# Performance work log

Measured on AMD Instinct MI355X. Metric: run time of the kernel, lower is better.

The kernel has to match this reference:

```python
import jax, jax.numpy as jnp
import numpy as np

EPS = 1e-8


def setup_inputs() -> dict:
    key = jax.random.key(0)
    k1, k2 = jax.random.split(key)
    N, D, K = 200000, 256, 64
    embeds = jax.random.normal(k1, (N, D), dtype=jnp.float32)
    init = jax.random.uniform(k2, (K, D), dtype=jnp.float32)  # torch.rand(K, n_h)
    beta = jnp.ones((1,), dtype=jnp.float32)
    return {"embeds": embeds, "init": init, "beta": beta, "num_iter": 11}


def reference(embeds, init, beta, num_iter):
    # embeds: [N, D], init: [K, D], beta: scalar temperature
    data_abs = jnp.linalg.norm(embeds, axis=1, keepdims=True)            # [N, 1]
    data_norm = embeds / jnp.maximum(data_abs, EPS)                      # [N, D]
    b = beta.reshape(())
    mu = init
    r = None
    for _ in range(num_iter):  # small fixed iteration count (default 11)
        mu_abs = jnp.linalg.norm(mu, axis=1, keepdims=True)              # [K, 1]
        mu_norm = mu / jnp.maximum(mu_abs, EPS)                          # [K, D]
        dist = data_norm @ mu_norm.T                                     # [N, K]
        r = jax.nn.softmax(b * dist, axis=1)                             # [N, K]
        cluster_r = r.sum(axis=0)                                        # [K]
        cluster_mean = r.T @ embeds                                      # [K, D]
        mu = cluster_mean / cluster_r[:, None]                           # diag(1/cluster_r) @ cluster_mean
    return mu, r
```

## Files before the change

### kernel.cpp

```cpp
#include <hip/hip_runtime.h>
#include <math.h>


#define N_ROWS 200000
#define DIM 256
#define KC 64
#define NUM_ITER 11
#define TR 64
#define NTILES (N_ROWS / TR)
#define EPSV 1e-8f
#define NB 256

typedef _Float16 half8 __attribute__((ext_vector_type(8)));
typedef _Float16 half4 __attribute__((ext_vector_type(4)));
typedef float f32x4 __attribute__((ext_vector_type(4)));

typedef __attribute__((address_space(3))) void as3_void;
typedef __attribute__((address_space(1))) void as1_void;

__device__ __forceinline__ void glds16(const void* g, void* l) {
  __builtin_amdgcn_global_load_lds((const as1_void*)g, (as3_void*)l, 16, 0, 0);
}

__device__ __forceinline__ float wave_reduce_sum(float v) {
#pragma unroll
  for (int off = 32; off > 0; off >>= 1) v += __shfl_xor(v, off, 64);
  return v;
}

__device__ __forceinline__ void barrier_lgkm_only() {
  __builtin_amdgcn_sched_barrier(0);
  asm volatile("s_waitcnt lgkmcnt(0)" ::: "memory");
  __builtin_amdgcn_s_barrier();
  __builtin_amdgcn_sched_barrier(0);
}


__global__ void rn_convert_kernel(const float* __restrict__ embeds,
                                  float* __restrict__ inv_norm,
                                  _Float16* __restrict__ Xh) {
  int gw = (blockIdx.x * blockDim.x + threadIdx.x) >> 6;
  int lane = threadIdx.x & 63;
  int nw = (gridDim.x * blockDim.x) >> 6;
  for (int row = gw; row < N_ROWS; row += nw) {
    float4 v = *(const float4*)(embeds + (size_t)row * DIM + 4 * lane);
    float s = v.x * v.x;
    s = fmaf(v.y, v.y, s); s = fmaf(v.z, v.z, s); s = fmaf(v.w, v.w, s);
    s = wave_reduce_sum(s);
    if (lane == 0) inv_norm[row] = 1.0f / fmaxf(sqrtf(s), EPSV);
    half4 h;
    h[0] = (_Float16)v.x; h[1] = (_Float16)v.y; h[2] = (_Float16)v.z; h[3] = (_Float16)v.w;
    *(half4*)(Xh + (size_t)row * DIM + 4 * lane) = h;
  }
}

__global__ void prep0_raw(const float* __restrict__ init, float* __restrict__ mu_raw,
                          float* __restrict__ mu_ssq) {
  int k = blockIdx.x, lane = threadIdx.x;
  float4 v = *(const float4*)(init + (size_t)k * DIM + 4 * lane);
  *(float4*)(mu_raw + (size_t)k * DIM + 4 * lane) = v;
  float s = v.x * v.x;
  s = fmaf(v.y, v.y, s); s = fmaf(v.z, v.z, s); s = fmaf(v.w, v.w, s);
#pragma unroll
  for (int off = 1; off < 16; off <<= 1) s += __shfl_xor(s, off, 64);
  if ((lane & 15) == 0) mu_ssq[k * 4 + (lane >> 4)] = s;
}

__device__ __forceinline__ void stage_row512_8(const _Float16* g, _Float16* l,
                                               int wid, int lane) {
#pragma unroll
  for (int ii = 0; ii < 4; ++ii) {
    int i = wid * 4 + ii;
    int row = i * 2 + (lane >> 5);
    int slot = (lane & 31) ^ (row & 7);
    glds16((const char*)g + row * 512 + slot * 16, (char*)l + i * 1024);
  }
}

template <int LAST>
__global__ __launch_bounds__(512, 2) void cluster_main8(
    const _Float16* __restrict__ Xh, const float* __restrict__ inv_norm,
    const float* __restrict__ beta, const float* __restrict__ mu_raw,
    const float* __restrict__ mu_ssq, float* __restrict__ part_cm,
    float* __restrict__ part_crt, float* __restrict__ r_out) {
  __shared__ alignas(16) _Float16 mu_lds[KC * DIM];
  __shared__ alignas(16) _Float16 x_lds[2][TR * DIM];
  __shared__ alignas(16) _Float16 xt_lds[DIM * TR];
  __shared__ alignas(16) _Float16 r_lds[KC * TR];
  __shared__ f32x4 dist_lds[16 * 64];
  __shared__ float cr_lds[4 * KC];

  const int tid = threadIdx.x, wid = tid >> 6, lane = tid & 63;
  const int l15 = lane & 15, h = lane >> 4;
  const int kh = wid >> 2, rg = wid & 3;
  const float b = beta[0];
  const int myrow = 16 * rg + l15;
  const int rb0 = blockIdx.x;

  stage_row512_8(Xh + (size_t)rb0 * TR * DIM, x_lds[0], wid, lane);

  if (tid < KC) {
    const float4 s4 = *(const float4*)&mu_ssq[4 * tid];
    cr_lds[tid] = 1.0f / fmaxf(sqrtf(s4.x + s4.y + s4.z + s4.w), EPSV);
  }
  __syncthreads();
  {
    const float4* mu_raw4 = (const float4*)mu_raw;
#pragma unroll
    for (int i = 0; i < 8; ++i) {
      const int idx = tid + 512 * i;
      const int cl = idx >> 6;
      const int dim0 = (idx & 63) * 4;
      float4 v = mu_raw4[idx];
      const float iv = cr_lds[cl];
      const int sw = dim0 ^ ((cl & 7) << 3);
      half4 hh;
      hh[0] = (_Float16)(v.x * iv); hh[1] = (_Float16)(v.y * iv);
      hh[2] = (_Float16)(v.z * iv); hh[3] = (_Float16)(v.w * iv);
      *(half4*)&mu_lds[cl * DIM + sw] = hh;
    }
  }
  f32x4 acc2[4][2] = {};
  float cr_acc[16] = {};
  __syncthreads();

  int p = 0;
  for (int rb = rb0; rb < NTILES; rb += NB, p ^= 1) {
    const int row0 = rb * TR;
    const int rbn = rb + NB;
    if (rbn < NTILES)
      stage_row512_8(Xh + (size_t)rbn * TR * DIM, x_lds[p ^ 1], wid, lane);

    f32x4 acc1[4] = {};
    const _Float16* xb = x_lds[p];
#pragma unroll
    for (int t = 0; t < 4; ++t) {
      const int kb = 128 * kh + 32 * t + 8 * h;
      half8 bx = *(const half8*)&xb[myrow * DIM + (kb ^ ((myrow & 7) << 3))];
#pragma unroll
      for (int m = 0; m < 4; ++m) {
        const int cl = 16 * m + l15;
        half8 am = *(const half8*)&mu_lds[cl * DIM + (kb ^ ((cl & 7) << 3))];
        acc1[m] = __builtin_amdgcn_mfma_f32_16x16x32_f16(am, bx, acc1[m], 0, 0, 0);
      }
    }
    if (kh) {
#pragma unroll
      for (int m = 0; m < 4; ++m) dist_lds[(rg * 4 + m) * 64 + lane] = acc1[m];
    }
    barrier_lgkm_only();

    if (!kh) {
#pragma unroll
      for (int m = 0; m < 4; ++m) {
        f32x4 o = dist_lds[(rg * 4 + m) * 64 + lane];
        acc1[m] += o;
      }
      const int xr = row0 + myrow;
      const float sc = b * inv_norm[xr];
#pragma unroll
      for (int m = 0; m < 4; ++m)
#pragma unroll
        for (int j = 0; j < 4; ++j) acc1[m][j] *= sc;
      float mx = -1e30f;
#pragma unroll
      for (int m = 0; m < 4; ++m)
#pragma unroll
        for (int j = 0; j < 4; ++j) mx = fmaxf(mx, acc1[m][j]);
      mx = fmaxf(mx, __shfl_xor(mx, 16));
      mx = fmaxf(mx, __shfl_xor(mx, 32));
      float esum = 0.f;
#pragma unroll
      for (int m = 0; m < 4; ++m)
#pragma unroll
        for (int j = 0; j < 4; ++j) {
          float e = __expf(acc1[m][j] - mx);
          acc1[m][j] = e;
          esum += e;
        }
      esum += __shfl_xor(esum, 16);
      esum += __shfl_xor(esum, 32);
      const float rcp = 1.0f / esum;
#pragma unroll
      for (int m = 0; m < 4; ++m) {
#pragma unroll
        for (int j = 0; j < 4; ++j) {
          const float rv = acc1[m][j] * rcp;
          acc1[m][j] = rv;
          const int cl = 16 * m + 4 * h + j;
          cr_acc[m * 4 + j] += rv;
          r_lds[cl * TR + (myrow ^ ((cl & 7) << 3))] = (_Float16)rv;
        }
        if (LAST)
          *(float4*)&r_out[(size_t)xr * KC + 16 * m + 4 * h] = *(float4*)&acc1[m];
      }
    } else {
      const int t8 = tid & 255;
      const int db = t8 >> 3;
      const int rb8 = t8 & 7;
      union U { uint4 v; unsigned u[4]; };
      U tin[8];
#pragma unroll
      for (int k2 = 0; k2 < 8; ++k2)
        tin[k2].v = *(const uint4*)&xb[(8 * rb8 + k2) * DIM + ((8 * db) ^ (k2 << 3))];
#pragma unroll
      for (int j = 0; j < 8; ++j) {
        const unsigned sel = (j & 1) ? 0x07060302u : 0x05040100u;
        U o;
#pragma unroll
        for (int m2 = 0; m2 < 4; ++m2)
          o.u[m2] = __builtin_amdgcn_perm(tin[2 * m2 + 1].u[j >> 1],
                                          tin[2 * m2].u[j >> 1], sel);
        *(uint4*)&xt_lds[(8 * db + j) * TR + 8 * (rb8 ^ j)] = o.v;
      }
    }

    barrier_lgkm_only();

#pragma unroll
    for (int t = 0; t < 2; ++t) {
      const int kb = 32 * t + 8 * h;
      half8 ar[4], bx2[2];
#pragma unroll
      for (int m = 0; m < 4; ++m) {
        const int cl = 16 * m + l15;
        ar[m] = *(const half8*)&r_lds[cl * TR + (kb ^ ((cl & 7) << 3))];
      }
#pragma unroll
      for (int n = 0; n < 2; ++n) {
        const int dm = 32 * wid + 16 * n + l15;
        bx2[n] = *(const half8*)&xt_lds[dm * TR + (kb ^ ((dm & 7) << 3))];
      }
#pragma unroll
      for (int m = 0; m < 4; ++m)
#pragma unroll
        for (int n = 0; n < 2; ++n)
          acc2[m][n] = __builtin_amdgcn_mfma_f32_16x16x32_f16(ar[m], bx2[n], acc2[m][n], 0, 0, 0);
    }
    __syncthreads();
  }

  float* pc = part_cm + (size_t)blockIdx.x * (KC * DIM);
#pragma unroll
  for (int m = 0; m < 4; ++m)
#pragma unroll
    for (int n = 0; n < 2; ++n)
#pragma unroll
      for (int j = 0; j < 4; ++j)
        pc[(16 * m + 4 * h + j) * DIM + 32 * wid + 16 * n + l15] = acc2[m][n][j];
  if (wid < 4) {
#pragma unroll
    for (int m = 0; m < 4; ++m)
#pragma unroll
      for (int j = 0; j < 4; ++j) {
        float v = cr_acc[m * 4 + j];
        v += __shfl_xor(v, 1); v += __shfl_xor(v, 2);
        v += __shfl_xor(v, 4); v += __shfl_xor(v, 8);
        if (l15 == 0) cr_lds[wid * KC + 16 * m + 4 * h + j] = v;
      }
  }
  __syncthreads();
  if (wid == 0)
    part_crt[(size_t)lane * NB + blockIdx.x] =
        cr_lds[lane] + cr_lds[KC + lane] + cr_lds[2 * KC + lane] + cr_lds[3 * KC + lane];
}

template <int FINAL>
__global__ void reduce_mu(const float* __restrict__ part_cm,
                          const float* __restrict__ part_crt,
                          float* __restrict__ mu_raw, float* __restrict__ mu_ssq,
                          float* __restrict__ mu_out) {
  const int cl = blockIdx.x, q = blockIdx.y;
  const int tid = threadIdx.x, wid = tid >> 6, lane = tid & 63;
  __shared__ float red2[4 * 64];
  __shared__ float cr4[4];
  float c = part_crt[(size_t)cl * NB + tid];
  c = wave_reduce_sum(c);
  if (lane == 0) cr4[wid] = c;
  float s = 0.f;
  const float* basep =
      part_cm + (size_t)(64 * wid) * (KC * DIM) + cl * DIM + 64 * q + lane;
#pragma unroll 8
  for (int i = 0; i < 64; ++i) s += basep[(size_t)i * (KC * DIM)];
  red2[wid * 64 + lane] = s;
  __syncthreads();
  if (wid == 0) {
    const float crv = cr4[0] + cr4[1] + cr4[2] + cr4[3];
    const float st = red2[lane] + red2[64 + lane] + red2[128 + lane] + red2[192 + lane];
    const float mu = st / crv;
    const int dim = 64 * q + lane;
    if (FINAL) {
      mu_out[cl * DIM + dim] = mu;
    } else {
      mu_raw[cl * DIM + dim] = mu;
      float ss = wave_reduce_sum(mu * mu);
      if (lane == 0) mu_ssq[cl * 4 + q] = ss;
    }
  }
}

__global__ void rownorm_v1(const float* __restrict__ embeds, float* __restrict__ inv_norm) {
  int gw = (blockIdx.x * blockDim.x + threadIdx.x) >> 6;
  int lane = threadIdx.x & 63;
  int nw = (gridDim.x * blockDim.x) >> 6;
  for (int row = gw; row < N_ROWS; row += nw) {
    const float* rp = embeds + (size_t)row * DIM;
    float s = 0.f;
#pragma unroll
    for (int j = 0; j < 4; ++j) { float v = rp[lane + 64 * j]; s = fmaf(v, v, s); }
    s = wave_reduce_sum(s);
    if (lane == 0) inv_norm[row] = 1.0f / fmaxf(sqrtf(s), EPSV);
  }
}
__global__ void prep0_v1(const float* __restrict__ init, float* __restrict__ muT) {
  int k = blockIdx.x, lane = threadIdx.x;
  const float* rp = init + k * DIM;
  float v[4]; float s = 0.f;
#pragma unroll
  for (int j = 0; j < 4; ++j) { v[j] = rp[lane + 64 * j]; s = fmaf(v[j], v[j], s); }
  s = wave_reduce_sum(s);
  float inv = 1.0f / fmaxf(sqrtf(s), EPSV);
#pragma unroll
  for (int j = 0; j < 4; ++j) muT[(lane + 64 * j) * KC + k] = v[j] * inv;
}
__device__ __forceinline__ float wave_reduce_max_v1(float v) {
#pragma unroll
  for (int off = 32; off > 0; off >>= 1) v = fmaxf(v, __shfl_xor(v, off, 64));
  return v;
}
template <int LAST>
__global__ __launch_bounds__(256, 1) void main_v1(
    const float* __restrict__ embeds, const float* __restrict__ inv_norm,
    const float* __restrict__ muT, const float* __restrict__ beta,
    float* __restrict__ part_cm, float* __restrict__ part_cr,
    float* __restrict__ r_out, int nb) {
  __shared__ float mu_l[DIM * KC];
  __shared__ float x_l[TR * DIM];
  __shared__ float r_l[TR * KC];
  __shared__ float cr_l[4 * KC];
  const int tid = threadIdx.x, wid = tid >> 6, lane = tid & 63;
  const float b = beta[0];
  {
    const float4* m4 = (const float4*)muT; float4* ml4 = (float4*)mu_l;
#pragma unroll
    for (int i = 0; i < 16; ++i) ml4[tid + i * 256] = m4[tid + i * 256];
  }
  float acc[64];
#pragma unroll
  for (int i = 0; i < 64; ++i) acc[i] = 0.f;
  float cr = 0.f;
  for (int rb = blockIdx.x; rb < NTILES; rb += nb) {
    const int row0 = rb * TR;
    __syncthreads();
    {
      const float4* x4 = (const float4*)(embeds + (size_t)row0 * DIM);
      float4* xl4 = (float4*)x_l;
#pragma unroll
      for (int i = 0; i < 16; ++i) xl4[tid + i * 256] = x4[tid + i * 256];
    }
    __syncthreads();
    float dist[16];
#pragma unroll
    for (int r = 0; r < 16; ++r) dist[r] = 0.f;
    const int rbase = wid * 16;
    for (int d = 0; d < DIM; d += 4) {
      float mv0 = mu_l[(d + 0) * KC + lane], mv1 = mu_l[(d + 1) * KC + lane];
      float mv2 = mu_l[(d + 2) * KC + lane], mv3 = mu_l[(d + 3) * KC + lane];
#pragma unroll
      for (int r = 0; r < 16; ++r) {
        float4 xv = *(const float4*)&x_l[(rbase + r) * DIM + d];
        dist[r] = fmaf(xv.x, mv0, dist[r]); dist[r] = fmaf(xv.y, mv1, dist[r]);
        dist[r] = fmaf(xv.z, mv2, dist[r]); dist[r] = fmaf(xv.w, mv3, dist[r]);
      }
    }
#pragma unroll
    for (int r = 0; r < 16; ++r) {
      const int row = rbase + r;
      float s = b * (dist[r] * inv_norm[row0 + row]);
      float m = wave_reduce_max_v1(s);
      float e = __expf(s - m);
      float sum = wave_reduce_sum(e);
      float rv = e * (1.0f / sum);
      cr += rv;
      r_l[row * KC + lane] = rv;
      if (LAST) r_out[(size_t)(row0 + row) * KC + lane] = rv;
    }
    __syncthreads();
    const int dbase = wid * 64;
    for (int row = 0; row < TR; ++row) {
      float rv = r_l[row * KC + lane];
#pragma unroll
      for (int dd = 0; dd < 64; dd += 4) {
        float4 xv = *(const float4*)&x_l[row * DIM + dbase + dd];
        acc[dd + 0] = fmaf(rv, xv.x, acc[dd + 0]); acc[dd + 1] = fmaf(rv, xv.y, acc[dd + 1]);
        acc[dd + 2] = fmaf(rv, xv.z, acc[dd + 2]); acc[dd + 3] = fmaf(rv, xv.w, acc[dd + 3]);
      }
    }
  }
  {
    float* pp = part_cm + ((size_t)blockIdx.x * KC + lane) * DIM + wid * 64;
#pragma unroll
    for (int dd = 0; dd < 64; dd += 4)
      *(float4*)&pp[dd] = make_float4(acc[dd], acc[dd + 1], acc[dd + 2], acc[dd + 3]);
    cr_l[wid * KC + lane] = cr;
  }
  __syncthreads();
  if (wid == 0) {
    float c = cr_l[lane] + cr_l[64 + lane] + cr_l[128 + lane] + cr_l[192 + lane];
    part_cr[(size_t)blockIdx.x * KC + lane] = c;
  }
}
template <int FINAL>
__global__ void reduce_v1(const float* __restrict__ part_cm, const float* __restrict__ part_cr,
                          float* __restrict__ muT, float* __restrict__ mu_out, int nb) {
  const int k = blockIdx.x, t = threadIdx.x;
  __shared__ float red[256];
  float s = 0.f;
  for (int bl = 0; bl < nb; ++bl) s += part_cm[((size_t)bl * KC + k) * DIM + t];
  float c = 0.f;
  for (int bl = t; bl < nb; bl += 256) c += part_cr[(size_t)bl * KC + k];
  red[t] = c; __syncthreads();
#pragma unroll
  for (int off = 128; off > 0; off >>= 1) { if (t < off) red[t] += red[t + off]; __syncthreads(); }
  const float crv = red[0]; __syncthreads();
  const float mu = s / crv;
  if (FINAL) { mu_out[k * DIM + t] = mu; return; }
  red[t] = mu * mu; __syncthreads();
#pragma unroll
  for (int off = 128; off > 0; off >>= 1) { if (t < off) red[t] += red[t + off]; __syncthreads(); }
  const float inv = 1.0f / fmaxf(sqrtf(red[0]), EPSV);
  muT[t * KC + k] = mu * inv;
}

extern "C" void kernel_launch(void* const* d_in, const int* in_sizes, int n_in,
                              void* d_out, int out_size, void* d_ws, size_t ws_size,
                              hipStream_t stream) {
  const float* embeds = (const float*)d_in[0];
  const float* init = (const float*)d_in[1];
  const float* beta = (const float*)d_in[2];
  float* out_mu = (float*)d_out;
  float* out_r = out_mu + KC * DIM;
  char* ws = (char*)d_ws;

  const size_t szX = (size_t)N_ROWS * DIM * 2;
  const size_t szInv = (size_t)N_ROWS * 4;
  const size_t szMuR = (size_t)KC * DIM * 4;
  const size_t szSsq = (size_t)KC * 4 * 4;
  const size_t szPC = (size_t)NB * KC * DIM * 4;
  const size_t szPR = (size_t)KC * NB * 4;
  const size_t need = szX + szInv + szMuR + szSsq + szPC + szPR;

  if (ws_size >= need) {
    char* pp = ws;
    _Float16* Xh = (_Float16*)pp; pp += szX;
    float* invn = (float*)pp; pp += szInv;
    float* mu_raw = (float*)pp; pp += szMuR;
    float* mu_ssq = (float*)pp; pp += szSsq;
    float* pcm = (float*)pp; pp += szPC;
    float* pcrt = (float*)pp;

    rn_convert_kernel<<<2048, 256, 0, stream>>>(embeds, invn, Xh);
    prep0_raw<<<KC, 64, 0, stream>>>(init, mu_raw, mu_ssq);
    for (int it = 0; it < NUM_ITER; ++it) {
      if (it > 0)
        reduce_mu<0><<<dim3(KC, 4), 256, 0, stream>>>(pcm, pcrt, mu_raw, mu_ssq, nullptr);
      if (it == NUM_ITER - 1)
        cluster_main8<1><<<NB, 512, 0, stream>>>(Xh, invn, beta, mu_raw, mu_ssq,
                                                 pcm, pcrt, out_r);
      else
        cluster_main8<0><<<NB, 512, 0, stream>>>(Xh, invn, beta, mu_raw, mu_ssq,
                                                 pcm, pcrt, out_r);
    }
    reduce_mu<1><<<dim3(KC, 4), 256, 0, stream>>>(pcm, pcrt, nullptr, nullptr, out_mu);
  } else {
    float* wsf = (float*)d_ws;
    float* muT = wsf;
    float* invn = muT + DIM * KC;
    size_t avail = ws_size / sizeof(float);
    size_t fixed = (size_t)DIM * KC + N_ROWS;
    size_t per_blk = (size_t)KC * DIM + KC;
    int nb = 256;
    if (avail > fixed) {
      size_t mx = (avail - fixed) / per_blk;
      if (mx < 256) nb = (int)mx;
    } else nb = 1;
    if (nb < 1) nb = 1;
    float* pcm = invn + N_ROWS;
    float* pcr = pcm + (size_t)nb * KC * DIM;

    rownorm_v1<<<2048, 256, 0, stream>>>(embeds, invn);
    prep0_v1<<<KC, 64, 0, stream>>>(init, muT);
    for (int it = 0; it < NUM_ITER; ++it) {
      if (it > 0) reduce_v1<0><<<KC, 256, 0, stream>>>(pcm, pcr, muT, nullptr, nb);
      if (it == NUM_ITER - 1)
        main_v1<1><<<nb, 256, 0, stream>>>(embeds, invn, muT, beta, pcm, pcr, out_r, nb);
      else
        main_v1<0><<<nb, 256, 0, stream>>>(embeds, invn, muT, beta, pcm, pcr, nullptr, nb);
    }
    reduce_v1<1><<<KC, 256, 0, stream>>>(pcm, pcr, muT, out_mu, nb);
  }
}
```

Measured before the change: 517.0 us.

## Triple-buffer X tiles, transpose in place, give GEMM1 full K per wave

The main cluster kernel moves from double to triple buffering of X tiles, prefetching two tiles ahead and using explicit vmcnt waits in place of a full syncthreads at the end of each tile. The first GEMM is now done entirely by waves 0-3 over the full 256-dim reduction, which removes the split-K dist_lds exchange. Waves 4-7 meanwhile load the tile for transposition and write the transposed data back into the same buffer, so the separate xt_lds array is no longer needed. The prep0 kernel is folded into the convert kernel to save a launch. The risks are load imbalance between the two wave groups, possible hazards from the in-place overwrite, and a different LDS footprint that may affect occupancy.

Result: slower. 581.3 us (+12.4%).

```diff
diff --git a/kernel.cpp b/kernel.cpp
--- a/kernel.cpp
+++ b/kernel.cpp
@@ -35,10 +35,26 @@
   __builtin_amdgcn_sched_barrier(0);
 }
 
-
 __global__ void rn_convert_kernel(const float* __restrict__ embeds,
                                   float* __restrict__ inv_norm,
-                                  _Float16* __restrict__ Xh) {
+                                  _Float16* __restrict__ Xh,
+                                  const float* __restrict__ init,
+                                  float* __restrict__ mu_raw,
+                                  float* __restrict__ mu_ssq) {
+  if (blockIdx.x == 0) {
+    const int c = threadIdx.x >> 2, qq = threadIdx.x & 3;
+    const float4* src = (const float4*)(init + (size_t)c * DIM + 64 * qq);
+    float4* dst = (float4*)(mu_raw + (size_t)c * DIM + 64 * qq);
+    float ss = 0.f;
+#pragma unroll
+    for (int i = 0; i < 16; ++i) {
+      float4 v = src[i];
+      dst[i] = v;
+      ss = fmaf(v.x, v.x, ss); ss = fmaf(v.y, v.y, ss);
+      ss = fmaf(v.z, v.z, ss); ss = fmaf(v.w, v.w, ss);
+    }
+    mu_ssq[c * 4 + qq] = ss;
+  }
   int gw = (blockIdx.x * blockDim.x + threadIdx.x) >> 6;
   int lane = threadIdx.x & 63;
   int nw = (gridDim.x * blockDim.x) >> 6;
@@ -54,18 +70,6 @@
   }
 }
 
-__global__ void prep0_raw(const float* __restrict__ init, float* __restrict__ mu_raw,
-                          float* __restrict__ mu_ssq) {
-  int k = blockIdx.x, lane = threadIdx.x;
-  float4 v = *(const float4*)(init + (size_t)k * DIM + 4 * lane);
-  *(float4*)(mu_raw + (size_t)k * DIM + 4 * lane) = v;
-  float s = v.x * v.x;
-  s = fmaf(v.y, v.y, s); s = fmaf(v.z, v.z, s); s = fmaf(v.w, v.w, s);
-#pragma unroll
-  for (int off = 1; off < 16; off <<= 1) s += __shfl_xor(s, off, 64);
-  if ((lane & 15) == 0) mu_ssq[k * 4 + (lane >> 4)] = s;
-}
-
 __device__ __forceinline__ void stage_row512_8(const _Float16* g, _Float16* l,
                                                int wid, int lane) {
 #pragma unroll
@@ -84,26 +88,24 @@
     const float* __restrict__ mu_ssq, float* __restrict__ part_cm,
     float* __restrict__ part_crt, float* __restrict__ r_out) {
   __shared__ alignas(16) _Float16 mu_lds[KC * DIM];
-  __shared__ alignas(16) _Float16 x_lds[2][TR * DIM];
-  __shared__ alignas(16) _Float16 xt_lds[DIM * TR];
+  __shared__ alignas(16) _Float16 x_lds[3][TR * DIM];
   __shared__ alignas(16) _Float16 r_lds[KC * TR];
-  __shared__ f32x4 dist_lds[16 * 64];
   __shared__ float cr_lds[4 * KC];
 
   const int tid = threadIdx.x, wid = tid >> 6, lane = tid & 63;
   const int l15 = lane & 15, h = lane >> 4;
-  const int kh = wid >> 2, rg = wid & 3;
   const float b = beta[0];
-  const int myrow = 16 * rg + l15;
+  const int myrow = 16 * (wid & 3) + l15;
   const int rb0 = blockIdx.x;
 
   stage_row512_8(Xh + (size_t)rb0 * TR * DIM, x_lds[0], wid, lane);
+  stage_row512_8(Xh + (size_t)(rb0 + NB) * TR * DIM, x_lds[1], wid, lane);
 
   if (tid < KC) {
     const float4 s4 = *(const float4*)&mu_ssq[4 * tid];
     cr_lds[tid] = 1.0f / fmaxf(sqrtf(s4.x + s4.y + s4.z + s4.w), EPSV);
   }
-  __syncthreads();
+  barrier_lgkm_only();
   {
     const float4* mu_raw4 = (const float4*)mu_raw;
 #pragma unroll
@@ -120,43 +122,44 @@
       *(half4*)&mu_lds[cl * DIM + sw] = hh;
     }
   }
+  asm volatile("s_waitcnt vmcnt(4)" ::: "memory");
+  barrier_lgkm_only();
+
   f32x4 acc2[4][2] = {};
   float cr_acc[16] = {};
-  __syncthreads();
-
-  int p = 0;
-  for (int rb = rb0; rb < NTILES; rb += NB, p ^= 1) {
-    const int row0 = rb * TR;
-    const int rbn = rb + NB;
-    if (rbn < NTILES)
-      stage_row512_8(Xh + (size_t)rbn * TR * DIM, x_lds[p ^ 1], wid, lane);
+  int idx3 = 0;
+  for (int rb = rb0; rb < NTILES; rb += NB) {
+    _Float16* xb = x_lds[idx3];
+    const int i2 = (idx3 + 2 >= 3) ? idx3 - 1 : idx3 + 2;
+    const bool have1 = (rb + NB < NTILES), have2 = (rb + 2 * NB < NTILES);
+    if (!LAST && have2)
+      stage_row512_8(Xh + (size_t)(rb + 2 * NB) * TR * DIM, x_lds[i2], wid, lane);
 
     f32x4 acc1[4] = {};
-    const _Float16* xb = x_lds[p];
-#pragma unroll
-    for (int t = 0; t < 4; ++t) {
-      const int kb = 128 * kh + 32 * t + 8 * h;
-      half8 bx = *(const half8*)&xb[myrow * DIM + (kb ^ ((myrow & 7) << 3))];
-#pragma unroll
-      for (int m = 0; m < 4; ++m) {
-        const int cl = 16 * m + l15;
-        half8 am = *(const half8*)&mu_lds[cl * DIM + (kb ^ ((cl & 7) << 3))];
-        acc1[m] = __builtin_amdgcn_mfma_f32_16x16x32_f16(am, bx, acc1[m], 0, 0, 0);
-      }
-    }
-    if (kh) {
-#pragma unroll
-      for (int m = 0; m < 4; ++m) dist_lds[(rg * 4 + m) * 64 + lane] = acc1[m];
+    uint4 tin[8];
+    if (wid < 4) {
+#pragma unroll
+      for (int t = 0; t < 8; ++t) {
+        const int kb = 32 * t + 8 * h;
+        half8 bx = *(const half8*)&xb[myrow * DIM + (kb ^ ((myrow & 7) << 3))];
+#pragma unroll
+        for (int m = 0; m < 4; ++m) {
+          const int cl = 16 * m + l15;
+          half8 am = *(const half8*)&mu_lds[cl * DIM + (kb ^ ((cl & 7) << 3))];
+          acc1[m] = __builtin_amdgcn_mfma_f32_16x16x32_f16(am, bx, acc1[m], 0, 0, 0);
+        }
+      }
+    } else {
+      const int t8 = tid & 255;
+      const int db = t8 >> 3, rb8 = t8 & 7;
+#pragma unroll
+      for (int k2 = 0; k2 < 8; ++k2)
+        tin[k2] = *(const uint4*)&xb[(8 * rb8 + k2) * DIM + ((8 * db) ^ (k2 << 3))];
     }
     barrier_lgkm_only();
 
-    if (!kh) {
-#pragma unroll
-      for (int m = 0; m < 4; ++m) {
-        f32x4 o = dist_lds[(rg * 4 + m) * 64 + lane];
-        acc1[m] += o;
-      }
-      const int xr = row0 + myrow;
+    if (wid < 4) {
+      const int xr = rb * TR + myrow;
       const float sc = b * inv_norm[xr];
 #pragma unroll
       for (int m = 0; m < 4; ++m)
@@ -196,25 +199,21 @@
       }
     } else {
       const int t8 = tid & 255;
-      const int db = t8 >> 3;
-      const int rb8 = t8 & 7;
+      const int db = t8 >> 3, rb8 = t8 & 7;
       union U { uint4 v; unsigned u[4]; };
-      U tin[8];
-#pragma unroll
-      for (int k2 = 0; k2 < 8; ++k2)
-        tin[k2].v = *(const uint4*)&xb[(8 * rb8 + k2) * DIM + ((8 * db) ^ (k2 << 3))];
 #pragma unroll
       for (int j = 0; j < 8; ++j) {
         const unsigned sel = (j & 1) ? 0x07060302u : 0x05040100u;
         U o;
 #pragma unroll
         for (int m2 = 0; m2 < 4; ++m2)
-          o.u[m2] = __builtin_amdgcn_perm(tin[2 * m2 + 1].u[j >> 1],
-                                          tin[2 * m2].u[j >> 1], sel);
-        *(uint4*)&xt_lds[(8 * db + j) * TR + 8 * (rb8 ^ j)] = o.v;
-      }
-    }
-
+          o.u[m2] = __builtin_amdgcn_perm(((const unsigned*)&tin[2 * m2 + 1])[j >> 1],
+                                          ((const unsigned*)&tin[2 * m2])[j >> 1], sel);
+        *(uint4*)&xb[(8 * db + j) * TR + 8 * (rb8 ^ j)] = o.v;
+      }
+    }
+    if (LAST && have2)
+      stage_row512_8(Xh + (size_t)(rb + 2 * NB) * TR * DIM, x_lds[i2], wid, lane);
     barrier_lgkm_only();
 
 #pragma unroll
@@ -229,7 +228,7 @@
 #pragma unroll
       for (int n = 0; n < 2; ++n) {
         const int dm = 32 * wid + 16 * n + l15;
-        bx2[n] = *(const half8*)&xt_lds[dm * TR + (kb ^ ((dm & 7) << 3))];
+        bx2[n] = *(const half8*)&xb[dm * TR + (kb ^ ((dm & 7) << 3))];
       }
 #pragma unroll
       for (int m = 0; m < 4; ++m)
@@ -237,7 +236,13 @@
         for (int n = 0; n < 2; ++n)
           acc2[m][n] = __builtin_amdgcn_mfma_f32_16x16x32_f16(ar[m], bx2[n], acc2[m][n], 0, 0, 0);
     }
-    __syncthreads();
+
+    if (have1) {
+      if (have2) asm volatile("s_waitcnt vmcnt(4)" ::: "memory");
+      else       asm volatile("s_waitcnt vmcnt(0)" ::: "memory");
+      barrier_lgkm_only();
+    }
+    idx3 = (idx3 + 1 == 3) ? 0 : idx3 + 1;
   }
 
   float* pc = part_cm + (size_t)blockIdx.x * (KC * DIM);
@@ -459,8 +464,7 @@
     float* pcm = (float*)pp; pp += szPC;
     float* pcrt = (float*)pp;
 
-    rn_convert_kernel<<<2048, 256, 0, stream>>>(embeds, invn, Xh);
-    prep0_raw<<<KC, 64, 0, stream>>>(init, mu_raw, mu_ssq);
+    rn_convert_kernel<<<2048, 256, 0, stream>>>(embeds, invn, Xh, init, mu_raw, mu_ssq);
     for (int it = 0; it < NUM_ITER; ++it) {
       if (it > 0)
         reduce_mu<0><<<dim3(KC, 4), 256, 0, stream>>>(pcm, pcrt, mu_raw, mu_ssq, nullptr);
```

## Halve row tile, double blocks, keep normalized centroids in registers

Applied to the files above, without the earlier changes.

Reworks the main clustering kernel to 256-thread blocks processing 32-row tiles across 512 blocks, with each wave holding its normalized half-precision centroid fragments in registers instead of a shared-memory copy. The transpose and swizzle patterns are adjusted for the smaller tile, and the reduction kernel now sums twice as many partial blocks. The init copy and norm computation are folded into the row-norm conversion kernel to drop one launch. This trades lower LDS use and more parallelism for higher register pressure and a larger partial-sum reduction.

Result: slower. 943.4 us (+82.5%).

```diff
diff --git a/kernel.cpp b/kernel.cpp
--- a/kernel.cpp
+++ b/kernel.cpp
@@ -6,10 +6,10 @@
 #define DIM 256
 #define KC 64
 #define NUM_ITER 11
-#define TR 64
-#define NTILES (N_ROWS / TR)
+#define TR2 32
+#define NT2 (N_ROWS / TR2)
 #define EPSV 1e-8f
-#define NB 256
+#define NB2 512
 
 typedef _Float16 half8 __attribute__((ext_vector_type(8)));
 typedef _Float16 half4 __attribute__((ext_vector_type(4)));
@@ -35,10 +35,26 @@
   __builtin_amdgcn_sched_barrier(0);
 }
 
-
 __global__ void rn_convert_kernel(const float* __restrict__ embeds,
                                   float* __restrict__ inv_norm,
-                                  _Float16* __restrict__ Xh) {
+                                  _Float16* __restrict__ Xh,
+                                  const float* __restrict__ init,
+                                  float* __restrict__ mu_raw,
+                                  float* __restrict__ mu_ssq) {
+  if (blockIdx.x == 0) {
+    const int c = threadIdx.x >> 2, qq = threadIdx.x & 3;
+    const float4* src = (const float4*)(init + (size_t)c * DIM + 64 * qq);
+    float4* dst = (float4*)(mu_raw + (size_t)c * DIM + 64 * qq);
+    float ss = 0.f;
+#pragma unroll
+    for (int i = 0; i < 16; ++i) {
+      float4 v = src[i];
+      dst[i] = v;
+      ss = fmaf(v.x, v.x, ss); ss = fmaf(v.y, v.y, ss);
+      ss = fmaf(v.z, v.z, ss); ss = fmaf(v.w, v.w, ss);
+    }
+    mu_ssq[c * 4 + qq] = ss;
+  }
   int gw = (blockIdx.x * blockDim.x + threadIdx.x) >> 6;
   int lane = threadIdx.x & 63;
   int nw = (gridDim.x * blockDim.x) >> 6;
@@ -54,20 +70,8 @@
   }
 }
 
-__global__ void prep0_raw(const float* __restrict__ init, float* __restrict__ mu_raw,
-                          float* __restrict__ mu_ssq) {
-  int k = blockIdx.x, lane = threadIdx.x;
-  float4 v = *(const float4*)(init + (size_t)k * DIM + 4 * lane);
-  *(float4*)(mu_raw + (size_t)k * DIM + 4 * lane) = v;
-  float s = v.x * v.x;
-  s = fmaf(v.y, v.y, s); s = fmaf(v.z, v.z, s); s = fmaf(v.w, v.w, s);
-#pragma unroll
-  for (int off = 1; off < 16; off <<= 1) s += __shfl_xor(s, off, 64);
-  if ((lane & 15) == 0) mu_ssq[k * 4 + (lane >> 4)] = s;
-}
-
-__device__ __forceinline__ void stage_row512_8(const _Float16* g, _Float16* l,
-                                               int wid, int lane) {
+__device__ __forceinline__ void stage_tile32(const _Float16* g, _Float16* l,
+                                             int wid, int lane) {
 #pragma unroll
   for (int ii = 0; ii < 4; ++ii) {
     int i = wid * 4 + ii;
@@ -78,71 +82,68 @@
 }
 
 template <int LAST>
-__global__ __launch_bounds__(512, 2) void cluster_main8(
+__global__ __launch_bounds__(256, 2) void cluster_main4(
     const _Float16* __restrict__ Xh, const float* __restrict__ inv_norm,
     const float* __restrict__ beta, const float* __restrict__ mu_raw,
     const float* __restrict__ mu_ssq, float* __restrict__ part_cm,
     float* __restrict__ part_crt, float* __restrict__ r_out) {
-  __shared__ alignas(16) _Float16 mu_lds[KC * DIM];
-  __shared__ alignas(16) _Float16 x_lds[2][TR * DIM];
-  __shared__ alignas(16) _Float16 xt_lds[DIM * TR];
-  __shared__ alignas(16) _Float16 r_lds[KC * TR];
-  __shared__ f32x4 dist_lds[16 * 64];
-  __shared__ float cr_lds[4 * KC];
+  __shared__ alignas(16) _Float16 x_lds[2][TR2 * DIM];
+  __shared__ alignas(16) _Float16 xt_lds[DIM * TR2];
+  __shared__ alignas(16) _Float16 r_lds[KC * TR2];
+  __shared__ alignas(16) f32x4 dist_lds[8 * 64];
+  __shared__ float cr_lds[2 * KC];
 
   const int tid = threadIdx.x, wid = tid >> 6, lane = tid & 63;
   const int l15 = lane & 15, h = lane >> 4;
-  const int kh = wid >> 2, rg = wid & 3;
+  const int kh = wid >> 1, rg = wid & 1;
   const float b = beta[0];
   const int myrow = 16 * rg + l15;
   const int rb0 = blockIdx.x;
 
-  stage_row512_8(Xh + (size_t)rb0 * TR * DIM, x_lds[0], wid, lane);
+  stage_tile32(Xh + (size_t)rb0 * TR2 * DIM, x_lds[0], wid, lane);
 
   if (tid < KC) {
     const float4 s4 = *(const float4*)&mu_ssq[4 * tid];
     cr_lds[tid] = 1.0f / fmaxf(sqrtf(s4.x + s4.y + s4.z + s4.w), EPSV);
   }
   __syncthreads();
-  {
-    const float4* mu_raw4 = (const float4*)mu_raw;
-#pragma unroll
-    for (int i = 0; i < 8; ++i) {
-      const int idx = tid + 512 * i;
-      const int cl = idx >> 6;
-      const int dim0 = (idx & 63) * 4;
-      float4 v = mu_raw4[idx];
+
+  half8 amreg[4][4];
+#pragma unroll
+  for (int t = 0; t < 4; ++t) {
+    const int kb = 128 * kh + 32 * t + 8 * h;
+#pragma unroll
+    for (int m = 0; m < 4; ++m) {
+      const int cl = 16 * m + l15;
+      const float* q = mu_raw + (size_t)cl * DIM + kb;
+      const float4 lo = *(const float4*)q;
+      const float4 hi = *(const float4*)(q + 4);
       const float iv = cr_lds[cl];
-      const int sw = dim0 ^ ((cl & 7) << 3);
-      half4 hh;
-      hh[0] = (_Float16)(v.x * iv); hh[1] = (_Float16)(v.y * iv);
-      hh[2] = (_Float16)(v.z * iv); hh[3] = (_Float16)(v.w * iv);
-      *(half4*)&mu_lds[cl * DIM + sw] = hh;
-    }
-  }
-  f32x4 acc2[4][2] = {};
+      half8 r;
+      r[0] = (_Float16)(lo.x * iv); r[1] = (_Float16)(lo.y * iv);
+      r[2] = (_Float16)(lo.z * iv); r[3] = (_Float16)(lo.w * iv);
+      r[4] = (_Float16)(hi.x * iv); r[5] = (_Float16)(hi.y * iv);
+      r[6] = (_Float16)(hi.z * iv); r[7] = (_Float16)(hi.w * iv);
+      amreg[t][m] = r;
+    }
+  }
+
+  f32x4 acc2[4][4] = {};
   float cr_acc[16] = {};
-  __syncthreads();
-
   int p = 0;
-  for (int rb = rb0; rb < NTILES; rb += NB, p ^= 1) {
-    const int row0 = rb * TR;
-    const int rbn = rb + NB;
-    if (rbn < NTILES)
-      stage_row512_8(Xh + (size_t)rbn * TR * DIM, x_lds[p ^ 1], wid, lane);
+  for (int rb = rb0; rb < NT2; rb += NB2, p ^= 1) {
+    _Float16* xb = x_lds[p];
+    if (rb + NB2 < NT2)
+      stage_tile32(Xh + (size_t)(rb + NB2) * TR2 * DIM, x_lds[p ^ 1], wid, lane);
 
     f32x4 acc1[4] = {};
-    const _Float16* xb = x_lds[p];
 #pragma unroll
     for (int t = 0; t < 4; ++t) {
       const int kb = 128 * kh + 32 * t + 8 * h;
       half8 bx = *(const half8*)&xb[myrow * DIM + (kb ^ ((myrow & 7) << 3))];
 #pragma unroll
-      for (int m = 0; m < 4; ++m) {
-        const int cl = 16 * m + l15;
-        half8 am = *(const half8*)&mu_lds[cl * DIM + (kb ^ ((cl & 7) << 3))];
-        acc1[m] = __builtin_amdgcn_mfma_f32_16x16x32_f16(am, bx, acc1[m], 0, 0, 0);
-      }
+      for (int m = 0; m < 4; ++m)
+        acc1[m] = __builtin_amdgcn_mfma_f32_16x16x32_f16(amreg[t][m], bx, acc1[m], 0, 0, 0);
     }
     if (kh) {
 #pragma unroll
@@ -152,11 +153,8 @@
 
     if (!kh) {
 #pragma unroll
-      for (int m = 0; m < 4; ++m) {
-        f32x4 o = dist_lds[(rg * 4 + m) * 64 + lane];
-        acc1[m] += o;
-      }
-      const int xr = row0 + myrow;
+      for (int m = 0; m < 4; ++m) acc1[m] += dist_lds[(rg * 4 + m) * 64 + lane];
+      const int xr = rb * TR2 + myrow;
       const float sc = b * inv_norm[xr];
 #pragma unroll
       for (int m = 0; m < 4; ++m)
@@ -189,15 +187,14 @@
           acc1[m][j] = rv;
           const int cl = 16 * m + 4 * h + j;
           cr_acc[m * 4 + j] += rv;
-          r_lds[cl * TR + (myrow ^ ((cl & 7) << 3))] = (_Float16)rv;
+          r_lds[cl * TR2 + (myrow ^ ((cl & 3) << 3))] = (_Float16)rv;
         }
         if (LAST)
           *(float4*)&r_out[(size_t)xr * KC + 16 * m + 4 * h] = *(float4*)&acc1[m];
       }
     } else {
-      const int t8 = tid & 255;
-      const int db = t8 >> 3;
-      const int rb8 = t8 & 7;
+      const int t8 = tid & 127;
+      const int db = t8 >> 2, rb8 = t8 & 3;
       union U { uint4 v; unsigned u[4]; };
       U tin[8];
 #pragma unroll
@@ -205,36 +202,35 @@
         tin[k2].v = *(const uint4*)&xb[(8 * rb8 + k2) * DIM + ((8 * db) ^ (k2 << 3))];
 #pragma unroll
       for (int j = 0; j < 8; ++j) {
-        const unsigned sel = (j & 1) ? 0x07060302u : 0x05040100u;
+        const int jp = j ^ (db & 7);
+        const unsigned sel = (jp & 1) ? 0x07060302u : 0x05040100u;
         U o;
 #pragma unroll
         for (int m2 = 0; m2 < 4; ++m2)
-          o.u[m2] = __builtin_amdgcn_perm(tin[2 * m2 + 1].u[j >> 1],
-                                          tin[2 * m2].u[j >> 1], sel);
-        *(uint4*)&xt_lds[(8 * db + j) * TR + 8 * (rb8 ^ j)] = o.v;
-      }
-    }
-
+          o.u[m2] = __builtin_amdgcn_perm(tin[2 * m2 + 1].u[jp >> 1],
+                                          tin[2 * m2].u[jp >> 1], sel);
+        *(uint4*)&xt_lds[(8 * db + jp) * TR2 + 8 * (rb8 ^ (jp & 3))] = o.v;
+      }
+    }
     barrier_lgkm_only();
 
-#pragma unroll
-    for (int t = 0; t < 2; ++t) {
-      const int kb = 32 * t + 8 * h;
-      half8 ar[4], bx2[2];
+    {
+      const int kb = 8 * h;
+      half8 ar[4], bx2[4];
 #pragma unroll
       for (int m = 0; m < 4; ++m) {
         const int cl = 16 * m + l15;
-        ar[m] = *(const half8*)&r_lds[cl * TR + (kb ^ ((cl & 7) << 3))];
-      }
-#pragma unroll
-      for (int n = 0; n < 2; ++n) {
-        const int dm = 32 * wid + 16 * n + l15;
-        bx2[n] = *(const half8*)&xt_lds[dm * TR + (kb ^ ((dm & 7) << 3))];
+        ar[m] = *(const half8*)&r_lds[cl * TR2 + (kb ^ ((cl & 3) << 3))];
+      }
+#pragma unroll
+      for (int n = 0; n < 4; ++n) {
+        const int dm = 64 * wid + 16 * n + l15;
+        bx2[n] = *(const half8*)&xt_lds[dm * TR2 + (kb ^ ((dm & 3) << 3))];
       }
 #pragma unroll
       for (int m = 0; m < 4; ++m)
 #pragma unroll
-        for (int n = 0; n < 2; ++n)
+        for (int n = 0; n < 4; ++n)
           acc2[m][n] = __builtin_amdgcn_mfma_f32_16x16x32_f16(ar[m], bx2[n], acc2[m][n], 0, 0, 0);
     }
     __syncthreads();
@@ -244,11 +240,11 @@
 #pragma unroll
   for (int m = 0; m < 4; ++m)
 #pragma unroll
-    for (int n = 0; n < 2; ++n)
+    for (int n = 0; n < 4; ++n)
 #pragma unroll
       for (int j = 0; j < 4; ++j)
-        pc[(16 * m + 4 * h + j) * DIM + 32 * wid + 16 * n + l15] = acc2[m][n][j];
-  if (wid < 4) {
+        pc[(16 * m + 4 * h + j) * DIM + 64 * wid + 16 * n + l15] = acc2[m][n][j];
+  if (kh == 0) {
 #pragma unroll
     for (int m = 0; m < 4; ++m)
 #pragma unroll
@@ -261,8 +257,8 @@
   }
   __syncthreads();
   if (wid == 0)
-    part_crt[(size_t)lane * NB + blockIdx.x] =
-        cr_lds[lane] + cr_lds[KC + lane] + cr_lds[2 * KC + lane] + cr_lds[3 * KC + lane];
+    part_crt[(size_t)lane * NB2 + blockIdx.x] =
+        cr_lds[lane] + cr_lds[KC + lane];
 }
 
 template <int FINAL>
@@ -274,14 +270,15 @@
   const int tid = threadIdx.x, wid = tid >> 6, lane = tid & 63;
   __shared__ float red2[4 * 64];
   __shared__ float cr4[4];
-  float c = part_crt[(size_t)cl * NB + tid];
+  float c = part_crt[(size_t)cl * NB2 + tid] +
+            part_crt[(size_t)cl * NB2 + 256 + tid];
   c = wave_reduce_sum(c);
   if (lane == 0) cr4[wid] = c;
   float s = 0.f;
   const float* basep =
-      part_cm + (size_t)(64 * wid) * (KC * DIM) + cl * DIM + 64 * q + lane;
+      part_cm + (size_t)(128 * wid) * (KC * DIM) + cl * DIM + 64 * q + lane;
 #pragma unroll 8
-  for (int i = 0; i < 64; ++i) s += basep[(size_t)i * (KC * DIM)];
+  for (int i = 0; i < 128; ++i) s += basep[(size_t)i * (KC * DIM)];
   red2[wid * 64 + lane] = s;
   __syncthreads();
   if (wid == 0) {
@@ -299,6 +296,8 @@
   }
 }
 
+#define TR 64
+#define NTILES (N_ROWS / TR)
 __global__ void rownorm_v1(const float* __restrict__ embeds, float* __restrict__ inv_norm) {
   int gw = (blockIdx.x * blockDim.x + threadIdx.x) >> 6;
   int lane = threadIdx.x & 63;
@@ -446,8 +445,8 @@
   const size_t szInv = (size_t)N_ROWS * 4;
   const size_t szMuR = (size_t)KC * DIM * 4;
   const size_t szSsq = (size_t)KC * 4 * 4;
-  const size_t szPC = (size_t)NB * KC * DIM * 4;
-  const size_t szPR = (size_t)KC * NB * 4;
+  const size_t szPC = (size_t)NB2 * KC * DIM * 4;
+  const size_t szPR = (size_t)KC * NB2 * 4;
   const size_t need = szX + szInv + szMuR + szSsq + szPC + szPR;
 
   if (ws_size >= need) {
@@ -459,17 +458,16 @@
     float* pcm = (float*)pp; pp += szPC;
     float* pcrt = (float*)pp;
 
-    rn_convert_kernel<<<2048, 256, 0, stream>>>(embeds, invn, Xh);
-    prep0_raw<<<KC, 64, 0, stream>>>(init, mu_raw, mu_ssq);
+    rn_convert_kernel<<<2048, 256, 0, stream>>>(embeds, invn, Xh, init, mu_raw, mu_ssq);
     for (int it = 0; it < NUM_ITER; ++it) {
       if (it > 0)
         reduce_mu<0><<<dim3(KC, 4), 256, 0, stream>>>(pcm, pcrt, mu_raw, mu_ssq, nullptr);
       if (it == NUM_ITER - 1)
-        cluster_main8<1><<<NB, 512, 0, stream>>>(Xh, invn, beta, mu_raw, mu_ssq,
-                                                 pcm, pcrt, out_r);
+        cluster_main4<1><<<NB2, 256, 0, stream>>>(Xh, invn, beta, mu_raw, mu_ssq,
+                                                  pcm, pcrt, out_r);
       else
-        cluster_main8<0><<<NB, 512, 0, stream>>>(Xh, invn, beta, mu_raw, mu_ssq,
-                                                 pcm, pcrt, out_r);
+        cluster_main4<0><<<NB2, 256, 0, stream>>>(Xh, invn, beta, mu_raw, mu_ssq,
+                                                  pcm, pcrt, out_r);
     }
     reduce_mu<1><<<dim3(KC, 4), 256, 0, stream>>>(pcm, pcrt, nullptr, nullptr, out_mu);
   } else {
```
